# Optimization experiments

Hardware: AMD Instinct MI355X
Metric: run time of the kernel (lower is better)

Reference implementation:

```python
import jax, jax.numpy as jnp
import numpy as np


def _cdist(queries, data):
    # Euclidean distance matrix [m, n], matching torch.cdist(p=2)
    q2 = jnp.sum(queries * queries, axis=1)[:, None]
    d2 = jnp.sum(data * data, axis=1)[None, :]
    sq = q2 + d2 - 2.0 * (queries @ data.T)
    return jnp.sqrt(jnp.maximum(sq, 0.0))


def setup_inputs() -> dict:
    key = jax.random.key(0)
    k1, k2 = jax.random.split(key)
    data = jax.random.normal(k1, (16384, 3), dtype=jnp.float32)
    queries = jax.random.normal(k2, (16384, 3), dtype=jnp.float32)
    return {"data": data, "queries": queries, "n_neigbor": 32}


def reference(data, queries, n_neigbor):
    m = queries.shape[0]
    n = data.shape[0]
    dists = _cdist(queries, data)                      # [m, n]
    sorted_dist = jnp.sort(dists, axis=1)              # full row sort, as in original
    k = sorted_dist[:, n_neigbor]                      # (n_neigbor)-th smallest distance
    in_nbr = dists < k[:, None]                        # strictly-less -> exactly n_neigbor True per row (no ties)
    # nonzero() in the original emits column indices in ascending order per row.
    # Replicate with fixed shapes: map non-neighbors to sentinel n, sort, keep first n_neigbor.
    cols = jnp.where(in_nbr, jnp.arange(n, dtype=jnp.int64)[None, :], jnp.int64(n))
    neighbors_index = jnp.sort(cols, axis=1)[:, :n_neigbor].reshape(-1)  # [m * n_neigbor]
    counts = jnp.sum(in_nbr.astype(jnp.int64), axis=1)
    splits = jnp.concatenate([jnp.zeros((1,), dtype=jnp.int64), jnp.cumsum(counts)])  # [m+1]
    return neighbors_index, splits
```

## Files before the change

kernel.cpp:

```cpp
#include <hip/hip_runtime.h>
#include <stdint.h>

typedef unsigned long long u64;
typedef unsigned int u32;

#define NQ 16384
#define ND 16384
#define KNB 32
#define KK 33
#define SPLITS_BASE (NQ * KNB)
#define CAP 512
#define NRR (CAP / 64)
#define NWQ 2
#define G 36
#define G3 (G*G*G)
#define SCB ((G3 + 255) / 256)
#define FINF (__int_as_float(0x7f800000))


template<int BITS>
__device__ __forceinline__ int wave_sum_small(int v) {
    int tot = 0;
    #pragma unroll
    for (int b = 0; b < BITS; ++b)
        tot += (int)__popcll(__ballot((v >> b) & 1)) << b;
    return tot;
}
__device__ __forceinline__ float wave_max_f(float v) {
    #pragma unroll
    for (int s = 1; s < 64; s <<= 1) v = fmaxf(v, __shfl_xor(v, s, 64));
    return v;
}
__device__ __forceinline__ int wave_excl_prefix(int v, int lane) {
    int x = v;
    #pragma unroll
    for (int s = 1; s < 64; s <<= 1) {
        const int y = __shfl_up(x, s, 64);
        if (lane >= s) x += y;
    }
    return x - v;
}
__device__ __forceinline__ int iclamp(int v, int lo, int hi) {
    return v < lo ? lo : (v > hi ? hi : v);
}
__device__ __forceinline__ u32 fenc(float f) {
    const u32 u = __float_as_uint(f);
    return (u & 0x80000000u) ? ~u : (u | 0x80000000u);
}
__device__ __forceinline__ float fdec(u32 e) {
    const u32 u = (e & 0x80000000u) ? (e & 0x7fffffffu) : ~e;
    return __uint_as_float(u);
}

__device__ __forceinline__ float bisect_rank8(const float (&r)[NRR], int rank) {
    u32 lo = 0u, hi = 0x7f800000u;
    #pragma unroll 1
    while (lo < hi) {
        const u32 mid = (lo + hi) >> 1;
        const float pv = __uint_as_float(mid);
        int c = 0;
        #pragma unroll
        for (int j = 0; j < NRR; ++j) c += (r[j] <= pv) ? 1 : 0;
        const int tot = wave_sum_small<4>(c);
        if (tot >= rank) hi = mid; else lo = mid + 1;
    }
    return __uint_as_float(hi);
}

__device__ __forceinline__ void bitonic128(float& v0, float& v1, int lane) {
    #pragma unroll
    for (int k = 2; k <= 128; k <<= 1) {
        #pragma unroll
        for (int j = k >> 1; j >= 1; j >>= 1) {
            if (j >= 64) {
                const float a = fminf(v0, v1), b = fmaxf(v0, v1);
                v0 = a; v1 = b;
            } else {
                const float o0 = __shfl_xor(v0, j, 64);
                const float o1 = __shfl_xor(v1, j, 64);
                const bool bj = ((lane & j) == 0);
                const bool up0 = (k == 128) ? true : ((lane & k) == 0);
                const bool up1 = (k == 128) ? true : ((k == 64) ? false : ((lane & k) == 0));
                v0 = (bj == up0) ? fminf(v0, o0) : fmaxf(v0, o0);
                v1 = (bj == up1) ? fminf(v1, o1) : fmaxf(v1, o1);
            }
        }
    }
}

__device__ __forceinline__ void pool_prune(float* kp, u32* ip, int& cnt, float& Tk,
                                           int lane, u64 lt) {
    float m = FINF;
    #pragma unroll 1
    for (int j = lane; j < cnt; j += 64) m = fminf(m, kp[j]);
    const float M = wave_max_f(m);
    int nc = 0;
    #pragma unroll 1
    for (int j0 = 0; j0 < cnt; j0 += 64) {
        const int j = j0 + lane;
        const bool val = j < cnt;
        float k = FINF; u32 id = 0;
        if (val) { k = kp[j]; id = ip[j]; }
        const bool keep = val && (k <= M);
        const u64 mask = __ballot(keep);
        if (keep) {
            const int s = nc + (int)__popcll(mask & lt);
            kp[s] = k; ip[s] = id;
        }
        nc += (int)__popcll(mask);
    }
    cnt = nc; Tk = M;
}

__device__ __forceinline__ void pool_hard_prune(float* kp, u32* ip, int& cnt,
                                                int lane, u64 lt) {
    float r[NRR];
    #pragma unroll
    for (int j = 0; j < NRR; ++j) {
        const int s = j * 64 + lane;
        r[j] = (s < cnt) ? kp[s] : FINF;
    }
    const float v = bisect_rank8(r, 64);
    int nc = 0, eqs = 0;
    #pragma unroll 1
    for (int j0 = 0; j0 < cnt; j0 += 64) {
        const int j = j0 + lane;
        const bool val = j < cnt;
        float k = FINF; u32 id = 0;
        if (val) { k = kp[j]; id = ip[j]; }
        const bool lt_v = val && (k < v);
        const bool eq_v = val && (k == v);
        const u64 mlt = __ballot(lt_v);
        const u64 meq = __ballot(eq_v);
        const int poplt = (int)__popcll(mlt);
        const int popeq = (int)__popcll(meq);
        if (lt_v) { const int s = nc + (int)__popcll(mlt & lt); kp[s] = k; ip[s] = id; }
        if (eq_v) {
            const int pe = (int)__popcll(meq & lt);
            if (eqs + pe < 64) { const int s = nc + poplt + pe; kp[s] = k; ip[s] = id; }
        }
        int kept_eq = popeq;
        if (eqs + popeq > 64) kept_eq = (64 - eqs > 0) ? (64 - eqs) : 0;
        nc += poplt + kept_eq;
        eqs += popeq;
    }
    cnt = nc;
}

__device__ __forceinline__ void grid_geom(const u32* bbe, float& mnx, float& mny, float& mnz,
                                          float& hx, float& hy, float& hz) {
    mnx = fdec(bbe[0]); mny = fdec(bbe[1]); mnz = fdec(bbe[2]);
    const float mxx = -fdec(bbe[3]), mxy = -fdec(bbe[4]), mxz = -fdec(bbe[5]);
    hx = fmaxf((mxx - mnx) * (1.0f / G), 1e-20f);
    hy = fmaxf((mxy - mny) * (1.0f / G), 1e-20f);
    hz = fmaxf((mxz - mnz) * (1.0f / G), 1e-20f);
}

__device__ __forceinline__ u32 cell_of(const u32* bbe, float x, float y, float z) {
    float mnx, mny, mnz, hx, hy, hz;
    grid_geom(bbe, mnx, mny, mnz, hx, hy, hz);
    const int cx = iclamp((int)((x - mnx) / hx), 0, G-1);
    const int cy = iclamp((int)((y - mny) / hy), 0, G-1);
    const int cz = iclamp((int)((z - mnz) / hz), 0, G-1);
    return (u32)((cz * G + cy) * G + cx);
}

__global__ __launch_bounds__(256) void bbox_kernel(const float* __restrict__ data,
                                                   u32* __restrict__ bbe,
                                                   u32* __restrict__ hist) {
    const int i = blockIdx.x * 256 + threadIdx.x;
    for (int h = i; h < G3; h += ND) hist[h] = 0u;
    const int lane = threadIdx.x & 63;
    const float x = data[3*i], y = data[3*i+1], z = data[3*i+2];
    float mnx = x, mny = y, mnz = z, nx = -x, ny = -y, nz = -z;
    #pragma unroll
    for (int s = 1; s < 64; s <<= 1) {
        mnx = fminf(mnx, __shfl_xor(mnx, s, 64)); nx = fminf(nx, __shfl_xor(nx, s, 64));
        mny = fminf(mny, __shfl_xor(mny, s, 64)); ny = fminf(ny, __shfl_xor(ny, s, 64));
        mnz = fminf(mnz, __shfl_xor(mnz, s, 64)); nz = fminf(nz, __shfl_xor(nz, s, 64));
    }
    if (lane == 0) {
        atomicMin(&bbe[0], fenc(mnx)); atomicMin(&bbe[1], fenc(mny)); atomicMin(&bbe[2], fenc(mnz));
        atomicMin(&bbe[3], fenc(nx));  atomicMin(&bbe[4], fenc(ny));  atomicMin(&bbe[5], fenc(nz));
    }
}

__global__ __launch_bounds__(256) void cellid_hist(const float* __restrict__ data,
                                                   const u32* __restrict__ bbe,
                                                   u32* __restrict__ hist) {
    const int i = blockIdx.x * 256 + threadIdx.x;
    atomicAdd(&hist[cell_of(bbe, data[3*i], data[3*i+1], data[3*i+2])], 1u);
}

__global__ __launch_bounds__(256) void scan_partial(const u32* __restrict__ hist,
                                                    u32* __restrict__ cstart,
                                                    u32* __restrict__ bsum) {
    __shared__ u32 lds[256];
    const int t = threadIdx.x;
    const int i = blockIdx.x * 256 + t;
    const u32 v = (i < G3) ? hist[i] : 0u;
    lds[t] = v;
    __syncthreads();
    u32 x = v;
    for (int off = 1; off < 256; off *= 2) {
        const u32 add = (t >= off) ? lds[t - off] : 0u;
        __syncthreads();
        x += add; lds[t] = x;
        __syncthreads();
    }
    if (i < G3) cstart[i] = x - v;
    if (t == 255) bsum[blockIdx.x] = x;
}

__global__ __launch_bounds__(256) void scan_add(u32* __restrict__ cstart,
                                                u32* __restrict__ cursor,
                                                const u32* __restrict__ bsum) {
    __shared__ u32 lds[256];
    const int t = threadIdx.x;
    const u32 bv = (t < SCB) ? bsum[t] : 0u;
    lds[t] = bv;
    __syncthreads();
    u32 y = bv;
    for (int off = 1; off < 256; off *= 2) {
        const u32 add = (t >= off) ? lds[t - off] : 0u;
        __syncthreads();
        y += add; lds[t] = y;
        __syncthreads();
    }
    const u32 excl = lds[blockIdx.x] - ((blockIdx.x < SCB) ? bsum[blockIdx.x] : 0u);
    __syncthreads();
    const int i = blockIdx.x * 256 + t;
    if (i < G3) {
        const u32 val = cstart[i] + excl;
        cstart[i] = val; cursor[i] = val;
    }
    if (i == 0) cstart[G3] = (u32)ND;
}

__global__ __launch_bounds__(256) void scatter(const float* __restrict__ data,
                                               const u32* __restrict__ bbe,
                                               u32* __restrict__ cursor,
                                               float4* __restrict__ pts) {
    const int i = blockIdx.x * 256 + threadIdx.x;
    const float x = data[3*i], y = data[3*i+1], z = data[3*i+2];
    const u32 pos = atomicAdd(&cursor[cell_of(bbe, x, y, z)], 1u);
    pts[pos] = make_float4(x, y, z, __uint_as_float((u32)i));
}

__global__ __launch_bounds__(64 * NWQ) void knn_grid(const float4* __restrict__ pts,
                                                     const u32* __restrict__ cstart,
                                                     const float* __restrict__ queries,
                                                     const u32* __restrict__ bbe,
                                                     int* __restrict__ out_nb,
                                                     int* __restrict__ splits) {
    __shared__ float keyP[NWQ][CAP];
    __shared__ u32   idxP[NWQ][CAP];
    __shared__ int   accI[NWQ][KNB];

    const int lane = threadIdx.x & 63;
    const int wid  = threadIdx.x >> 6;
    const int q = blockIdx.x * NWQ + wid;
    const u64 lt = (1ull << lane) - 1ull;
    float* kp = keyP[wid];
    u32*   ip = idxP[wid];

    const float qx = queries[3*q], qy = queries[3*q+1], qz = queries[3*q+2];
    const float q2 = __fadd_rn(__fadd_rn(__fmul_rn(qx,qx), __fmul_rn(qy,qy)), __fmul_rn(qz,qz));

    float mnx, mny, mnz, hx, hy, hz;
    grid_geom(bbe, mnx, mny, mnz, hx, hy, hz);
    const float hmin = fminf(hx, fminf(hy, hz));
    const int cx = iclamp((int)((qx - mnx) / hx), 0, G-1);
    const int cy = iclamp((int)((qy - mny) / hy), 0, G-1);
    const int cz = iclamp((int)((qz - mnz) / hz), 0, G-1);

    float Tk = FINF;
    int cnt = 0;

    auto gather_batch = [&](int sA, int lA, int sB, int lB) {
        const int len = lA + lB;
        const int P = wave_excl_prefix(len, lane);
        const int T = __shfl(P + len, 63, 64);
        #pragma unroll 1
        for (int g0 = 0; g0 < T; g0 += 64) {
            const int pos = g0 + lane;
            const bool val = pos < T;
            int rsel = 0;
            #pragma unroll
            for (int st = 32; st >= 1; st >>= 1) {
                const int t = rsel + st;
                const int Pt = __shfl(P, t, 64);
                if (Pt <= pos) rsel = t;
            }
            const int Pr  = __shfl(P,  rsel, 64);
            const int sAr = __shfl(sA, rsel, 64);
            const int lAr = __shfl(lA, rsel, 64);
            const int sBr = __shfl(sB, rsel, 64);
            const int off = pos - Pr;
            const int pi = (off < lAr) ? (sAr + off) : (sBr + (off - lAr));
            float key = FINF; u32 oi = 0; bool acc = false;
            if (val) {
                const float4 w = pts[pi];
                oi = __float_as_uint(w.w);
                const float d2 = __fadd_rn(__fadd_rn(__fmul_rn(w.x,w.x), __fmul_rn(w.y,w.y)),
                                           __fmul_rn(w.z,w.z));
                const float dot = __fmaf_rn(qz, w.z, __fmaf_rn(qy, w.y, __fmul_rn(qx, w.x)));
                const float sq  = __fsub_rn(__fadd_rn(q2, d2), __fadd_rn(dot, dot));
                key = fmaxf(sq, 0.0f);
                acc = key <= Tk;
            }
            const u64 mask = __ballot(acc);
            if (mask) {
                if (acc) {
                    const int s = cnt + (int)__popcll(mask & lt);
                    kp[s] = key; ip[s] = oi;
                }
                cnt += (int)__popcll(mask);
                if (cnt > CAP - 64) {
                    pool_prune(kp, ip, cnt, Tk, lane, lt);
                    if (cnt > CAP - 64) pool_hard_prune(kp, ip, cnt, lane, lt);
                }
            }
        }
    };

    auto select33 = [&]() -> float {
        int guard = 0;
        while (cnt > 128 && guard < 2) { pool_prune(kp, ip, cnt, Tk, lane, lt); ++guard; }
        if (cnt <= 128) {
            float v0 = (lane < cnt) ? kp[lane] : FINF;
            float v1 = (64 + lane < cnt) ? kp[64 + lane] : FINF;
            bitonic128(v0, v1, lane);
            return __shfl(v0, KK - 1, 64);
        }
        float r[NRR];
        #pragma unroll
        for (int j = 0; j < NRR; ++j) {
            const int s = j * 64 + lane;
            r[j] = (s < cnt) ? kp[s] : FINF;
        }
        return bisect_rank8(r, KK);
    };

    int W = -1;
    while (cnt < KK && W < G) {
        ++W;
        const int side = 2*W + 1, nrows = side * side;
        for (int r0 = 0; r0 < nrows; r0 += 64) {
            const int rid = r0 + lane;
            int sA = 0, lA = 0, sB = 0, lB = 0;
            if (rid < nrows) {
                const int dz = rid / side - W, dy = rid % side - W;
                const int zz = cz + dz, yy = cy + dy;
                if (zz >= 0 && zz < G && yy >= 0 && yy < G) {
                    const int adz = dz < 0 ? -dz : dz;
                    const int ady = dy < 0 ? -dy : dy;
                    const int rb = (zz * G + yy) * G;
                    if (adz == W || ady == W) {
                        const int xlo = cx - W < 0 ? 0 : cx - W;
                        const int xhi = cx + W > G-1 ? G-1 : cx + W;
                        sA = (int)cstart[rb + xlo];
                        lA = (int)cstart[rb + xhi + 1] - sA;
                    } else {
                        const int xl = cx - W, xr = cx + W;
                        if (xl >= 0)   { sA = (int)cstart[rb + xl]; lA = (int)cstart[rb + xl + 1] - sA; }
                        if (xr <= G-1) { sB = (int)cstart[rb + xr]; lB = (int)cstart[rb + xr + 1] - sB; }
                    }
                }
            }
            gather_batch(sA, lA, sB, lB);
        }
    }

    const float k33b = select33();

    {
        int nc = 0;
        #pragma unroll 1
        for (int j0 = 0; j0 < cnt; j0 += 64) {
            const int j = j0 + lane;
            const bool val = j < cnt;
            float k = FINF; u32 id = 0;
            if (val) { k = kp[j]; id = ip[j]; }
            const bool keep = val && (k <= k33b);
            const u64 mask = __ballot(keep);
            if (keep) {
                const int s = nc + (int)__popcll(mask & lt);
                kp[s] = k; ip[s] = id;
            }
            nc += (int)__popcll(mask);
        }
        cnt = nc; Tk = k33b;
    }

    const float R2m = __fmaf_rn(k33b, 1.0002f, 1e-3f);
    if (!(R2m < (float)W * (float)W * hmin * hmin)) {
        const float Rm = sqrtf(R2m);
        const int Dz = (int)fminf(floorf(Rm / hz) + 1.0f, (float)G);
        const int Dy = (int)fminf(floorf(Rm / hy) + 1.0f, (float)G);
        const int sidey = 2*Dy + 1;
        const int nrows = (2*Dz + 1) * sidey;
        for (int r0 = 0; r0 < nrows; r0 += 64) {
            const int rid = r0 + lane;
            int sA = 0, lA = 0, sB = 0, lB = 0;
            if (rid < nrows) {
                const int dz = rid / sidey - Dz;
                const int dy = rid % sidey - Dy;
                const int zz = cz + dz, yy = cy + dy;
                if (zz >= 0 && zz < G && yy >= 0 && yy < G) {
                    const int adz = dz < 0 ? -dz : dz;
                    const int ady = dy < 0 ? -dy : dy;
                    const float mz = (adz >= 1) ? (float)(adz - 1) * hz : 0.0f;
                    const float my = (ady >= 1) ? (float)(ady - 1) * hy : 0.0f;
                    const float rowmin2 = mz*mz + my*my;
                    if (rowmin2 <= R2m) {
                        const int dxr = (int)fminf(floorf(sqrtf(R2m - rowmin2) / hx) + 1.0f, (float)G);
                        const int xlo = cx - dxr < 0 ? 0 : cx - dxr;
                        const int xhi = cx + dxr > G-1 ? G-1 : cx + dxr;
                        if (xlo <= xhi) {
                            const int rb = (zz * G + yy) * G;
                            if (adz <= W && ady <= W) {
                                const int xhiA = (cx - W - 1 < xhi) ? cx - W - 1 : xhi;
                                const int xloB = (cx + W + 1 > xlo) ? cx + W + 1 : xlo;
                                if (xlo <= xhiA) {
                                    sA = (int)cstart[rb + xlo];
                                    lA = (int)cstart[rb + xhiA + 1] - sA;
                                }
                                if (xloB <= xhi) {
                                    sB = (int)cstart[rb + xloB];
                                    lB = (int)cstart[rb + xhi + 1] - sB;
                                }
                            } else {
                                sA = (int)cstart[rb + xlo];
                                lA = (int)cstart[rb + xhi + 1] - sA;
                            }
                        }
                    }
                }
            }
            gather_batch(sA, lA, sB, lB);
        }
    }

    const float k33 = select33();

    const float kd = sqrtf(k33);
    float cut;
    if (!(kd > 0.0f)) {
        cut = -1.0f;
    } else {
        int bi = __float_as_int(__fmul_rn(kd, kd));
        #pragma unroll 1
        for (int s = 0; s < 8; ++s) {
            if (bi > 0 && sqrtf(__int_as_float(bi - 1)) >= kd) --bi; else break;
        }
        #pragma unroll 1
        for (int s = 0; s < 8; ++s) {
            if (sqrtf(__int_as_float(bi)) < kd) ++bi; else break;
        }
        cut = __int_as_float(bi);
    }

    int c = 0;
    #pragma unroll 1
    for (int j0 = 0; j0 < cnt; j0 += 64) {
        const int j = j0 + lane;
        const bool val = j < cnt;
        const float k = val ? kp[j] : FINF;
        const bool keep = val && (k < cut);
        const u64 mask = __ballot(keep);
        if (keep) {
            const int s = c + (int)__popcll(mask & lt);
            if (s < KNB) accI[wid][s] = (int)ip[j];
        }
        c += (int)__popcll(mask);
    }
    if (c > KNB) c = KNB;

    if (lane < KNB) {
        if (lane < c) {
            const int my = accI[wid][lane];
            int rank = 0;
            #pragma unroll 1
            for (int j = 0; j < KNB; ++j)
                if (j < c) rank += (accI[wid][j] < my) ? 1 : 0;
            out_nb[(size_t)q * KNB + rank] = my;
        } else {
            out_nb[(size_t)q * KNB + lane] = ND;
        }
    }
    if (lane == 0) splits[1 + q] = c;
}

__global__ __launch_bounds__(256) void knn_direct_kernel(const float* __restrict__ data,
                                                         const float* __restrict__ queries,
                                                         int* __restrict__ out_nb,
                                                         int* __restrict__ splits) {
    __shared__ float4 tile[1024];
    const int q = blockIdx.x * 256 + threadIdx.x;
    const float qx = queries[3*q], qy = queries[3*q+1], qz = queries[3*q+2];
    const float q2 = __fadd_rn(__fadd_rn(__fmul_rn(qx,qx), __fmul_rn(qy,qy)), __fmul_rn(qz,qz));
    float arrk[KK]; int arri[KK];
    for (int j = 0; j < KK; ++j) { arrk[j] = FINF; arri[j] = ND; }
    float cur_maxk = FINF;
    for (int t0 = 0; t0 < ND; t0 += 1024) {
        for (int p = threadIdx.x; p < 1024; p += 256) {
            const int g = t0 + p;
            const float x = data[3*g], y = data[3*g+1], z = data[3*g+2];
            const float d2 = __fadd_rn(__fadd_rn(__fmul_rn(x,x), __fmul_rn(y,y)), __fmul_rn(z,z));
            tile[p] = make_float4(x, y, z, d2);
        }
        __syncthreads();
        for (int p = 0; p < 1024; ++p) {
            const float4 dp = tile[p];
            const float dot = __fmaf_rn(qz, dp.z, __fmaf_rn(qy, dp.y, __fmul_rn(qx, dp.x)));
            const float sq  = __fsub_rn(__fadd_rn(q2, dp.w), __fadd_rn(dot, dot));
            const float key = fmaxf(sq, 0.0f);
            if (key < cur_maxk) {
                int mp = 0; float m = -1.0f;
                for (int j = 0; j < KK; ++j) if (arrk[j] > m) { m = arrk[j]; mp = j; }
                arrk[mp] = key; arri[mp] = t0 + p;
                m = -1.0f;
                for (int j = 0; j < KK; ++j) if (arrk[j] > m) m = arrk[j];
                cur_maxk = m;
            }
        }
        __syncthreads();
    }
    const float kdist = sqrtf(cur_maxk);
    int acc[KNB]; int c = 0;
    for (int j = 0; j < KK; ++j) {
        const float d = sqrtf(arrk[j]);
        if (d < kdist && c < KNB) acc[c++] = arri[j];
    }
    for (int a = 1; a < c; ++a) {
        const int v = acc[a]; int j = a;
        while (j > 0 && acc[j-1] > v) { acc[j] = acc[j-1]; --j; }
        acc[j] = v;
    }
    int* row = out_nb + (size_t)q * KNB;
    for (int j = 0; j < KNB; ++j) row[j] = (j < c) ? acc[j] : ND;
    splits[1 + q] = c;
}

__global__ __launch_bounds__(1024) void splits_scan_kernel(int* __restrict__ splits) {
    __shared__ int lds[1024];
    const int t = threadIdx.x;
    int v[16]; int s = 0;
    #pragma unroll
    for (int j = 0; j < 16; ++j) { v[j] = splits[1 + t*16 + j]; s += v[j]; }
    lds[t] = s;
    __syncthreads();
    for (int off = 1; off < 1024; off *= 2) {
        const int add = (t >= off) ? lds[t - off] : 0;
        __syncthreads();
        lds[t] += add;
        __syncthreads();
    }
    int run = lds[t] - s;
    #pragma unroll
    for (int j = 0; j < 16; ++j) { run += v[j]; splits[1 + t*16 + j] = run; }
    if (t == 0) splits[0] = 0;
}

extern "C" void kernel_launch(void* const* d_in, const int* in_sizes, int n_in,
                              void* d_out, int out_size, void* d_ws, size_t ws_size,
                              hipStream_t stream) {
    const float* data    = (const float*)d_in[0];
    const float* queries = (const float*)d_in[1];
    int* out    = (int*)d_out;
    int* splits = out + SPLITS_BASE;

    const size_t bb_off     = 0;
    const size_t hist_off   = 64;
    const size_t cstart_off = hist_off + (size_t)G3 * 4;
    const size_t cursor_off = cstart_off + (size_t)(G3 + 1) * 4;
    const size_t bsum_off   = cursor_off + (size_t)G3 * 4;
    size_t pts_off          = bsum_off + 256 * 4;
    pts_off = (pts_off + 255) & ~(size_t)255;
    const size_t need       = pts_off + (size_t)ND * 16;

    if (ws_size >= need) {
        u32*    bbe    = (u32*)((char*)d_ws + bb_off);
        u32*    hist   = (u32*)((char*)d_ws + hist_off);
        u32*    cstart = (u32*)((char*)d_ws + cstart_off);
        u32*    cursor = (u32*)((char*)d_ws + cursor_off);
        u32*    bsum   = (u32*)((char*)d_ws + bsum_off);
        float4* pts    = (float4*)((char*)d_ws + pts_off);

        hipMemsetAsync(bbe, 0xFF, 24, stream);
        hipLaunchKernelGGL(bbox_kernel, dim3(ND / 256), dim3(256), 0, stream, data, bbe, hist);
        hipLaunchKernelGGL(cellid_hist, dim3(ND / 256), dim3(256), 0, stream, data, bbe, hist);
        hipLaunchKernelGGL(scan_partial, dim3(SCB), dim3(256), 0, stream, hist, cstart, bsum);
        hipLaunchKernelGGL(scan_add, dim3(SCB), dim3(256), 0, stream, cstart, cursor, bsum);
        hipLaunchKernelGGL(scatter, dim3(ND / 256), dim3(256), 0, stream, data, bbe, cursor, pts);
        hipLaunchKernelGGL(knn_grid, dim3(NQ / NWQ), dim3(64 * NWQ), 0, stream,
                           pts, cstart, queries, bbe, out, splits);
    } else {
        hipLaunchKernelGGL(knn_direct_kernel, dim3(NQ / 256), dim3(256), 0, stream,
                           data, queries, out, splits);
    }
    hipLaunchKernelGGL(splits_scan_kernel, dim3(1), dim3(1024), 0, stream, splits);
}
```

Before: 118.9 us.

## Refine grid to 48 cells and pick search window by counting before gathering

```diff
diff --git a/kernel.cpp b/kernel.cpp
--- a/kernel.cpp
+++ b/kernel.cpp
@@ -12,9 +12,9 @@
 #define CAP 512
 #define NRR (CAP / 64)
 #define NWQ 2
-#define G 36
+#define G 48
 #define G3 (G*G*G)
-#define SCB ((G3 + 255) / 256)
+#define SCB ((G3 + 1023) / 1024)
 #define FINF (__int_as_float(0x7f800000))
 
 
@@ -192,44 +192,44 @@
     atomicAdd(&hist[cell_of(bbe, data[3*i], data[3*i+1], data[3*i+2])], 1u);
 }
 
-__global__ __launch_bounds__(256) void scan_partial(const u32* __restrict__ hist,
-                                                    u32* __restrict__ cstart,
-                                                    u32* __restrict__ bsum) {
-    __shared__ u32 lds[256];
+__global__ __launch_bounds__(1024) void scan_partial(const u32* __restrict__ hist,
+                                                     u32* __restrict__ cstart,
+                                                     u32* __restrict__ bsum) {
+    __shared__ u32 lds[1024];
     const int t = threadIdx.x;
-    const int i = blockIdx.x * 256 + t;
+    const int i = blockIdx.x * 1024 + t;
     const u32 v = (i < G3) ? hist[i] : 0u;
     lds[t] = v;
     __syncthreads();
     u32 x = v;
-    for (int off = 1; off < 256; off *= 2) {
+    for (int off = 1; off < 1024; off *= 2) {
         const u32 add = (t >= off) ? lds[t - off] : 0u;
         __syncthreads();
         x += add; lds[t] = x;
         __syncthreads();
     }
     if (i < G3) cstart[i] = x - v;
-    if (t == 255) bsum[blockIdx.x] = x;
-}
-
-__global__ __launch_bounds__(256) void scan_add(u32* __restrict__ cstart,
-                                                u32* __restrict__ cursor,
-                                                const u32* __restrict__ bsum) {
-    __shared__ u32 lds[256];
+    if (t == 1023) bsum[blockIdx.x] = x;
+}
+
+__global__ __launch_bounds__(1024) void scan_add(u32* __restrict__ cstart,
+                                                 u32* __restrict__ cursor,
+                                                 const u32* __restrict__ bsum) {
+    __shared__ u32 lds[1024];
     const int t = threadIdx.x;
     const u32 bv = (t < SCB) ? bsum[t] : 0u;
     lds[t] = bv;
     __syncthreads();
     u32 y = bv;
-    for (int off = 1; off < 256; off *= 2) {
+    for (int off = 1; off < 1024; off *= 2) {
         const u32 add = (t >= off) ? lds[t - off] : 0u;
         __syncthreads();
         y += add; lds[t] = y;
         __syncthreads();
     }
-    const u32 excl = lds[blockIdx.x] - ((blockIdx.x < SCB) ? bsum[blockIdx.x] : 0u);
+    const u32 excl = lds[blockIdx.x] - bsum[blockIdx.x];
     __syncthreads();
-    const int i = blockIdx.x * 256 + t;
+    const int i = blockIdx.x * 1024 + t;
     if (i < G3) {
         const u32 val = cstart[i] + excl;
         cstart[i] = val; cursor[i] = val;
@@ -342,33 +342,48 @@
         return bisect_rank8(r, KK);
     };
 
-    int W = -1;
-    while (cnt < KK && W < G) {
-        ++W;
+    int W = 0;
+    {
+        int ccount = 0;
+        while (ccount < KK && W < G) {
+            W = (W < 4) ? W + 1 : ((2 * W <= G) ? 2 * W : G);
+            const int side = 2*W + 1, nrows = side * side;
+            ccount = 0;
+            for (int r0 = 0; r0 < nrows; r0 += 64) {
+                const int rid = r0 + lane;
+                int len = 0;
+                if (rid < nrows) {
+                    const int dz = rid / side - W, dy = rid % side - W;
+                    const int zz = cz + dz, yy = cy + dy;
+                    if (zz >= 0 && zz < G && yy >= 0 && yy < G) {
+                        const int xlo = cx - W < 0 ? 0 : cx - W;
+                        const int xhi = cx + W > G-1 ? G-1 : cx + W;
+                        const int rb = (zz * G + yy) * G;
+                        len = (int)cstart[rb + xhi + 1] - (int)cstart[rb + xlo];
+                    }
+                }
+                ccount += wave_sum_small<6>(len < 63 ? len : 63);
+            }
+        }
+    }
+
+    {
         const int side = 2*W + 1, nrows = side * side;
         for (int r0 = 0; r0 < nrows; r0 += 64) {
             const int rid = r0 + lane;
-            int sA = 0, lA = 0, sB = 0, lB = 0;
+            int sA = 0, lA = 0;
             if (rid < nrows) {
                 const int dz = rid / side - W, dy = rid % side - W;
                 const int zz = cz + dz, yy = cy + dy;
                 if (zz >= 0 && zz < G && yy >= 0 && yy < G) {
-                    const int adz = dz < 0 ? -dz : dz;
-                    const int ady = dy < 0 ? -dy : dy;
+                    const int xlo = cx - W < 0 ? 0 : cx - W;
+                    const int xhi = cx + W > G-1 ? G-1 : cx + W;
                     const int rb = (zz * G + yy) * G;
-                    if (adz == W || ady == W) {
-                        const int xlo = cx - W < 0 ? 0 : cx - W;
-                        const int xhi = cx + W > G-1 ? G-1 : cx + W;
-                        sA = (int)cstart[rb + xlo];
-                        lA = (int)cstart[rb + xhi + 1] - sA;
-                    } else {
-                        const int xl = cx - W, xr = cx + W;
-                        if (xl >= 0)   { sA = (int)cstart[rb + xl]; lA = (int)cstart[rb + xl + 1] - sA; }
-                        if (xr <= G-1) { sB = (int)cstart[rb + xr]; lB = (int)cstart[rb + xr + 1] - sB; }
-                    }
+                    sA = (int)cstart[rb + xlo];
+                    lA = (int)cstart[rb + xhi + 1] - sA;
                 }
             }
-            gather_batch(sA, lA, sB, lB);
+            gather_batch(sA, lA, 0, 0);
         }
     }
 
@@ -576,7 +591,7 @@
     const size_t cstart_off = hist_off + (size_t)G3 * 4;
     const size_t cursor_off = cstart_off + (size_t)(G3 + 1) * 4;
     const size_t bsum_off   = cursor_off + (size_t)G3 * 4;
-    size_t pts_off          = bsum_off + 256 * 4;
+    size_t pts_off          = bsum_off + 1024 * 4;
     pts_off = (pts_off + 255) & ~(size_t)255;
     const size_t need       = pts_off + (size_t)ND * 16;
 
@@ -591,8 +606,8 @@
         hipMemsetAsync(bbe, 0xFF, 24, stream);
         hipLaunchKernelGGL(bbox_kernel, dim3(ND / 256), dim3(256), 0, stream, data, bbe, hist);
         hipLaunchKernelGGL(cellid_hist, dim3(ND / 256), dim3(256), 0, stream, data, bbe, hist);
-        hipLaunchKernelGGL(scan_partial, dim3(SCB), dim3(256), 0, stream, hist, cstart, bsum);
-        hipLaunchKernelGGL(scan_add, dim3(SCB), dim3(256), 0, stream, cstart, cursor, bsum);
+        hipLaunchKernelGGL(scan_partial, dim3(SCB), dim3(1024), 0, stream, hist, cstart, bsum);
+        hipLaunchKernelGGL(scan_add, dim3(SCB), dim3(1024), 0, stream, cstart, cursor, bsum);
         hipLaunchKernelGGL(scatter, dim3(ND / 256), dim3(256), 0, stream, data, bbe, cursor, pts);
         hipLaunchKernelGGL(knn_grid, dim3(NQ / NWQ), dim3(64 * NWQ), 0, stream,
                            pts, cstart, queries, bbe, out, splits);
```

After: 125.3 us. 5.3% more time.
